# Kernel optimization log

Measured on AMD Instinct MI355X. Metric: run time of the kernel, lower is better.

The kernel has to match this reference:

```python
import jax, jax.numpy as jnp
import numpy as np

VOCAB = 50257
D = 1024
EDGES = [0, 20000, 40000, VOCAB]  # cluster boundaries
HSZ = [1024, 256, 64]             # D // 4**i per cluster


def setup_inputs() -> dict:
    key = jax.random.key(0)
    ks = jax.random.split(key, 8)
    emb_input = jax.random.randint(ks[0], (8, 2048), 0, VOCAB, dtype=jnp.int64)
    inp = {"emb_input": emb_input}
    for i in range(3):
        vsz = EDGES[i + 1] - EDGES[i]
        h = HSZ[i]
        inp[f"emb{i}"] = jax.random.normal(ks[1 + 2 * i], (vsz, h), dtype=jnp.float32) * 0.02
        # nn.Linear(h, D, bias=False) weight has shape [D, h]
        inp[f"w{i}"] = jax.random.normal(ks[2 + 2 * i], (D, h), dtype=jnp.float32) * 0.02
    return inp


def reference(emb_input, emb0, w0, emb1, w1, emb2, w2):
    B, S = emb_input.shape
    idx = emb_input.reshape(-1)  # [N]
    clusters = [(emb0, w0), (emb1, w1), (emb2, w2)]
    out = jnp.zeros((idx.shape[0], D), dtype=jnp.float32)
    for i, (emb, w) in enumerate(clusters):
        lo, hi = EDGES[i], EDGES[i + 1]
        mask = (idx >= lo) & (idx < hi)                       # [N]
        local = jnp.clip(idx - lo, 0, emb.shape[0] - 1)       # in-range gather ids
        h = emb[local]                                        # [N, hsz_i]
        proj = jnp.einsum('nh,dh->nd', h, w)                  # [N, D]
        out = out + jnp.where(mask[:, None], proj, 0.0)
    return out.reshape(B, S, D)
```

## Files before the change

### kernel.cpp

```cpp
#include <hip/hip_runtime.h>
#include <hip/hip_bf16.h>
#include <stdint.h>

#define DOUT 1024
#define NMAX 16384

#define BM 256
#define BN 128
#define LDSBUF 49152
#define BOFFS 32768

typedef __attribute__((ext_vector_type(8))) short short8;
typedef __attribute__((ext_vector_type(4))) float floatx4;

__device__ __forceinline__ unsigned short f2bf(float f) {
  union { float f; uint32_t u; } v;
  v.f = f;
  return (unsigned short)((v.u + 0x7FFFu + ((v.u >> 16) & 1u)) >> 16);
}

__device__ __forceinline__ short8 cvt8(float4 a, float4 b) {
  __hip_bfloat162 p0 = __float22bfloat162_rn(make_float2(a.x, a.y));
  __hip_bfloat162 p1 = __float22bfloat162_rn(make_float2(a.z, a.w));
  __hip_bfloat162 p2 = __float22bfloat162_rn(make_float2(b.x, b.y));
  __hip_bfloat162 p3 = __float22bfloat162_rn(make_float2(b.z, b.w));
  union { __hip_bfloat162 h[4]; short8 s; } u;
  u.h[0] = p0; u.h[1] = p1; u.h[2] = p2; u.h[3] = p3;
  return u.s;
}

__global__ __launch_bounds__(256) void classify_cvt_kernel(
    const int* __restrict__ idx, int* __restrict__ cnt,
    int* __restrict__ bucket, int* __restrict__ blocal, int N,
    const float* __restrict__ w0, const float* __restrict__ w1,
    const float* __restrict__ w2, unsigned short* __restrict__ wb0,
    unsigned short* __restrict__ wb1, unsigned short* __restrict__ wb2) {
  if (blockIdx.x < 64) {
    int n = blockIdx.x * 256 + threadIdx.x;
    int lane = threadIdx.x & 63;
    int c = -1, v = 0;
    if (n < N) {
      v = idx[n];
      c = (v < 20000) ? 0 : ((v < 40000) ? 1 : 2);
    }
#pragma unroll
    for (int k = 0; k < 3; ++k) {
      unsigned long long m = __ballot(c == k);
      if (c == k) {
        int leader = __ffsll((unsigned long long)m) - 1;
        int base = 0;
        if (lane == leader) base = atomicAdd(&cnt[k], (int)__popcll(m));
        base = __shfl(base, leader);
        int rank = (int)__popcll(m & ((1ull << (unsigned)lane) - 1ull));
        int lo = (k == 0) ? 0 : (k == 1) ? 20000 : 40000;
        bucket[k * NMAX + base + rank] = n;
        blocal[k * NMAX + base + rank] = v - lo;
      }
    }
  } else {
    int i = (blockIdx.x - 64) * 256 + threadIdx.x;
    if (i >= 344064) return;
    const float4* src;
    ushort4* dst;
    if (i < 262144) {
      src = (const float4*)w0 + i;
      dst = (ushort4*)wb0 + i;
    } else if (i < 327680) {
      src = (const float4*)w1 + (i - 262144);
      dst = (ushort4*)wb1 + (i - 262144);
    } else {
      src = (const float4*)w2 + (i - 327680);
      dst = (ushort4*)wb2 + (i - 327680);
    }
    float4 v = *src;
    ushort4 o;
    o.x = f2bf(v.x); o.y = f2bf(v.y); o.z = f2bf(v.z); o.w = f2bf(v.w);
    *dst = o;
  }
}

__global__ __launch_bounds__(256) void gather_kernel(
    const float* __restrict__ emb0, const float* __restrict__ emb1,
    const float* __restrict__ emb2, const int* __restrict__ cnt,
    const int* __restrict__ blocal, unsigned short* __restrict__ Abf) {
  const int b = blockIdx.x;
  const int c0 = cnt[0], c1 = cnt[1], c2 = cnt[2];
  const float* emb;
  const int* bl;
  int H, count, baseRow, lg;
  size_t off;
  if (b < 4096) {
    emb = emb0; bl = blocal; H = 1024; count = c0; off = 0;
    baseRow = b * 4; lg = 6;
  } else if (b < 5120) {
    emb = emb1; bl = blocal + NMAX; H = 256; count = c1;
    off = (size_t)c0 * 1024; baseRow = (b - 4096) * 16; lg = 4;
  } else {
    emb = emb2; bl = blocal + 2 * NMAX; H = 64; count = c2;
    off = (size_t)c0 * 1024 + (size_t)c1 * 256; baseRow = (b - 5120) * 64; lg = 2;
  }
  const int tid = threadIdx.x;
  const int r = baseRow + (tid >> lg);
  if (r >= count) return;
  const int e = (tid & ((1 << lg) - 1)) * 16;
  const float* src = emb + (size_t)bl[r] * H + e;
  unsigned short* d = Abf + off + (size_t)r * H + e;
  float4 v0 = ((const float4*)src)[0];
  float4 v1 = ((const float4*)src)[1];
  float4 v2 = ((const float4*)src)[2];
  float4 v3 = ((const float4*)src)[3];
  *(short8*)d = cvt8(v0, v1);
  *(short8*)(d + 8) = cvt8(v2, v3);
}

template <int H>
__device__ __forceinline__ void gemm_body(
    const unsigned short* __restrict__ A, const unsigned short* __restrict__ B,
    int count, const int* __restrict__ bucket, float* __restrict__ out,
    char* lds, int* rowTok) {
  const int m0 = blockIdx.y * BM;
  if (m0 >= count) return;
  const int n0 = blockIdx.x * BN;
  constexpr int NT = H / 64;

  const int tid = threadIdx.x;
  const int wave = tid >> 6;
  const int lane = tid & 63;
  const int quad = lane >> 4;
  const int l16 = lane & 15;
  const int wm = wave & 3;
  const int wn = wave >> 2;

  if (tid < BM) {
    int m = m0 + tid;
    rowTok[tid] = (m < count) ? bucket[m] : -1;
  }

  const int dl = wave * 1024 + lane * 16;
  const int lswz = dl ^ (((dl >> 7) & 3) << 4);
  const int rW = lswz >> 6;
  const int ckW = (lswz >> 4) & 3;
  const char* Abyte = (const char*)A;
  const char* Bbyte = (const char*)B;
  const size_t aOff0 = ((size_t)(m0 + rW) * H) * 2 + ckW * 16;
  const size_t aOff1 = ((size_t)(m0 + 128 + rW) * H) * 2 + ckW * 16;
  const size_t bOff = ((size_t)(n0 + rW) * H) * 2 + ckW * 16;

  auto stage = [&](int kt, char* buf) {
    const int kb = kt * 128;
#pragma unroll
    for (int s = 0; s < 2; ++s) {
      __builtin_amdgcn_global_load_lds(
          (const __attribute__((address_space(1))) void*)(Abyte + aOff0 + kb + s * 64),
          (__attribute__((address_space(3))) void*)(buf + s * 16384 + wave * 1024),
          16, 0, 0);
      __builtin_amdgcn_global_load_lds(
          (const __attribute__((address_space(1))) void*)(Abyte + aOff1 + kb + s * 64),
          (__attribute__((address_space(3))) void*)(buf + s * 16384 + 8192 + wave * 1024),
          16, 0, 0);
      __builtin_amdgcn_global_load_lds(
          (const __attribute__((address_space(1))) void*)(Bbyte + bOff + kb + s * 64),
          (__attribute__((address_space(3))) void*)(buf + BOFFS + s * 8192 + wave * 1024),
          16, 0, 0);
    }
  };

  int offA[2][4], offB[2][4];
#pragma unroll
  for (int s = 0; s < 2; ++s) {
#pragma unroll
    for (int i = 0; i < 4; ++i) {
      int ba = (wm * 64 + i * 16 + l16) * 64 + quad * 16;
      offA[s][i] = s * 16384 + (ba ^ (((ba >> 7) & 3) << 4));
      int bb = (wn * 64 + i * 16 + l16) * 64 + quad * 16;
      offB[s][i] = BOFFS + s * 8192 + (bb ^ (((bb >> 7) & 3) << 4));
    }
  }

  if (NT >= 1) stage(0, lds);
  if (NT >= 2) stage(1, lds + LDSBUF);
  if (NT >= 3) stage(2, lds + 2 * LDSBUF);

  floatx4 acc[4][4];
#pragma unroll
  for (int i = 0; i < 4; ++i)
#pragma unroll
    for (int j = 0; j < 4; ++j) acc[i][j] = (floatx4){0.f, 0.f, 0.f, 0.f};

#pragma unroll
  for (int kt = 0; kt < NT; ++kt) {
    const int rem = NT - 1 - kt;
    if (rem >= 2)
      asm volatile("s_waitcnt vmcnt(12)" ::: "memory");
    else if (rem == 1)
      asm volatile("s_waitcnt vmcnt(6)" ::: "memory");
    else
      asm volatile("s_waitcnt vmcnt(0)" ::: "memory");
    asm volatile("s_barrier" ::: "memory");

    const char* buf = lds + (kt % 3) * LDSBUF;
#pragma unroll
    for (int ph = 0; ph < 4; ++ph) {
      const int mh = ph >> 1, nh = ph & 1;
      short8 a[2][2], b[2][2];
#pragma unroll
      for (int s = 0; s < 2; ++s)
#pragma unroll
        for (int i = 0; i < 2; ++i) {
          a[s][i] = *(const short8*)(buf + offA[s][mh * 2 + i]);
          b[s][i] = *(const short8*)(buf + offB[s][nh * 2 + i]);
        }
      __builtin_amdgcn_s_setprio(1);
#pragma unroll
      for (int s = 0; s < 2; ++s)
#pragma unroll
        for (int i = 0; i < 2; ++i)
#pragma unroll
          for (int j = 0; j < 2; ++j)
            acc[mh * 2 + i][nh * 2 + j] = __builtin_amdgcn_mfma_f32_16x16x32_bf16(
                a[s][i], b[s][j], acc[mh * 2 + i][nh * 2 + j], 0, 0, 0);
      __builtin_amdgcn_s_setprio(0);
    }
    asm volatile("s_barrier" ::: "memory");
    if (kt + 3 < NT) stage(kt + 3, lds + (kt % 3) * LDSBUF);
  }

  const int colBase = n0 + wn * 64 + l16;
#pragma unroll
  for (int mi = 0; mi < 4; ++mi) {
#pragma unroll
    for (int r = 0; r < 4; ++r) {
      int tok = rowTok[wm * 64 + mi * 16 + quad * 4 + r];
      if (tok >= 0) {
        float* o = out + (size_t)tok * DOUT + colBase;
#pragma unroll
        for (int ni = 0; ni < 4; ++ni) o[ni * 16] = acc[mi][ni][r];
      }
    }
  }
}

__global__ __launch_bounds__(512, 2) void gemm_pipe(
    const unsigned short* __restrict__ Abf,
    const unsigned short* __restrict__ wb0,
    const unsigned short* __restrict__ wb1,
    const unsigned short* __restrict__ wb2, const int* __restrict__ cnt,
    const int* __restrict__ bucket, float* __restrict__ out) {
  __shared__ __align__(16) char lds[3 * LDSBUF + BM * 4];
  int* rowTok = (int*)(lds + 3 * LDSBUF);

  const int z = blockIdx.z;
  const int c0 = cnt[0];
  const int c1 = cnt[1];
  if (z == 0)
    gemm_body<1024>(Abf, wb0, c0, bucket, out, lds, rowTok);
  else if (z == 1)
    gemm_body<256>(Abf + (size_t)c0 * 1024, wb1, c1, bucket + NMAX, out, lds,
                   rowTok);
  else
    gemm_body<64>(Abf + (size_t)c0 * 1024 + (size_t)c1 * 256, wb2, cnt[2],
                  bucket + 2 * NMAX, out, lds, rowTok);
}

extern "C" void kernel_launch(void* const* d_in, const int* in_sizes, int n_in,
                              void* d_out, int out_size, void* d_ws, size_t ws_size,
                              hipStream_t stream) {
  const int* idx = (const int*)d_in[0];
  const float* emb0 = (const float*)d_in[1];
  const float* w0 = (const float*)d_in[2];
  const float* emb1 = (const float*)d_in[3];
  const float* w1 = (const float*)d_in[4];
  const float* emb2 = (const float*)d_in[5];
  const float* w2 = (const float*)d_in[6];
  float* out = (float*)d_out;
  const int N = in_sizes[0];

  char* ws = (char*)d_ws;
  int* cnt = (int*)ws;
  int* bucket = (int*)(ws + 1024);
  int* blocal = bucket + 3 * NMAX;
  size_t off = 1024 + (size_t)6 * NMAX * 4;
  off = (off + 255) & ~(size_t)255;
  unsigned short* wb0 = (unsigned short*)(ws + off); off += (size_t)DOUT * 1024 * 2;
  unsigned short* wb1 = (unsigned short*)(ws + off); off += (size_t)DOUT * 256 * 2;
  unsigned short* wb2 = (unsigned short*)(ws + off); off += (size_t)DOUT * 64 * 2;
  off = (off + 255) & ~(size_t)255;
  unsigned short* Abf = (unsigned short*)(ws + off);
  off += (size_t)(NMAX + 256) * 1024 * 2;

  hipMemsetAsync(cnt, 0, 16 * sizeof(int), stream);

  classify_cvt_kernel<<<64 + 1344, 256, 0, stream>>>(
      idx, cnt, bucket, blocal, N, w0, w1, w2, wb0, wb1, wb2);

  gather_kernel<<<5376, 256, 0, stream>>>(emb0, emb1, emb2, cnt, blocal, Abf);

  dim3 grid(DOUT / BN, NMAX / BM, 3);
  gemm_pipe<<<grid, 512, 0, stream>>>(Abf, wb0, wb1, wb2, cnt, bucket, out);
}
```

Baseline: 197.7 us.

## Coalesce gather-convert loads, swizzle GEMM workgroup order, load all fragments before MFMAs

The gather/convert kernel now has each thread handle four strided float4 chunks instead of one contiguous 64-byte chunk, so neighbouring lanes read neighbouring addresses. The GEMM remaps its linear workgroup id so consecutive ids are spread across eight XCD groups, aiming for better L2 locality. The inner k-loop also loads all A/B fragments for the whole tile at once and then issues all 32 MFMAs in one prioritised block, replacing four phased load/compute steps. This raises register pressure and gives up LDS/MFMA interleaving. The remap assumes the workgroup count divides evenly by eight.

```diff
diff --git a/kernel.cpp b/kernel.cpp
--- a/kernel.cpp
+++ b/kernel.cpp
@@ -19,13 +19,11 @@
   return (unsigned short)((v.u + 0x7FFFu + ((v.u >> 16) & 1u)) >> 16);
 }
 
-__device__ __forceinline__ short8 cvt8(float4 a, float4 b) {
-  __hip_bfloat162 p0 = __float22bfloat162_rn(make_float2(a.x, a.y));
-  __hip_bfloat162 p1 = __float22bfloat162_rn(make_float2(a.z, a.w));
-  __hip_bfloat162 p2 = __float22bfloat162_rn(make_float2(b.x, b.y));
-  __hip_bfloat162 p3 = __float22bfloat162_rn(make_float2(b.z, b.w));
-  union { __hip_bfloat162 h[4]; short8 s; } u;
-  u.h[0] = p0; u.h[1] = p1; u.h[2] = p2; u.h[3] = p3;
+__device__ __forceinline__ ushort4 cvt4(float4 v) {
+  __hip_bfloat162 p0 = __float22bfloat162_rn(make_float2(v.x, v.y));
+  __hip_bfloat162 p1 = __float22bfloat162_rn(make_float2(v.z, v.w));
+  union { __hip_bfloat162 h[2]; ushort4 s; } u;
+  u.h[0] = p0; u.h[1] = p1;
   return u.s;
 }
 
@@ -102,15 +100,16 @@
   const int tid = threadIdx.x;
   const int r = baseRow + (tid >> lg);
   if (r >= count) return;
-  const int e = (tid & ((1 << lg) - 1)) * 16;
+  const int tpr = 1 << lg;
+  const int e = (tid & (tpr - 1)) * 4;
+  const int stride = tpr * 4;
   const float* src = emb + (size_t)bl[r] * H + e;
   unsigned short* d = Abf + off + (size_t)r * H + e;
-  float4 v0 = ((const float4*)src)[0];
-  float4 v1 = ((const float4*)src)[1];
-  float4 v2 = ((const float4*)src)[2];
-  float4 v3 = ((const float4*)src)[3];
-  *(short8*)d = cvt8(v0, v1);
-  *(short8*)(d + 8) = cvt8(v2, v3);
+#pragma unroll
+  for (int j = 0; j < 4; ++j) {
+    float4 v = *(const float4*)(src + j * stride);
+    *(ushort4*)(d + j * stride) = cvt4(v);
+  }
 }
 
 template <int H>
@@ -118,9 +117,16 @@
     const unsigned short* __restrict__ A, const unsigned short* __restrict__ B,
     int count, const int* __restrict__ bucket, float* __restrict__ out,
     char* lds, int* rowTok) {
-  const int m0 = blockIdx.y * BM;
+  const int nwg = gridDim.x * gridDim.y;
+  const int orig = blockIdx.y * gridDim.x + blockIdx.x;
+  const int q = nwg >> 3;
+  const int wg = (orig & 7) * q + (orig >> 3);
+  const int bx = wg % gridDim.x;
+  const int by = wg / gridDim.x;
+
+  const int m0 = by * BM;
   if (m0 >= count) return;
-  const int n0 = blockIdx.x * BN;
+  const int n0 = bx * BN;
   constexpr int NT = H / 64;
 
   const int tid = threadIdx.x;
@@ -199,28 +205,24 @@
     asm volatile("s_barrier" ::: "memory");
 
     const char* buf = lds + (kt % 3) * LDSBUF;
-#pragma unroll
-    for (int ph = 0; ph < 4; ++ph) {
-      const int mh = ph >> 1, nh = ph & 1;
-      short8 a[2][2], b[2][2];
-#pragma unroll
-      for (int s = 0; s < 2; ++s)
-#pragma unroll
-        for (int i = 0; i < 2; ++i) {
-          a[s][i] = *(const short8*)(buf + offA[s][mh * 2 + i]);
-          b[s][i] = *(const short8*)(buf + offB[s][nh * 2 + i]);
-        }
-      __builtin_amdgcn_s_setprio(1);
-#pragma unroll
-      for (int s = 0; s < 2; ++s)
-#pragma unroll
-        for (int i = 0; i < 2; ++i)
-#pragma unroll
-          for (int j = 0; j < 2; ++j)
-            acc[mh * 2 + i][nh * 2 + j] = __builtin_amdgcn_mfma_f32_16x16x32_bf16(
-                a[s][i], b[s][j], acc[mh * 2 + i][nh * 2 + j], 0, 0, 0);
-      __builtin_amdgcn_s_setprio(0);
-    }
+    short8 a[2][4], b[2][4];
+#pragma unroll
+    for (int s = 0; s < 2; ++s)
+#pragma unroll
+      for (int i = 0; i < 4; ++i) {
+        a[s][i] = *(const short8*)(buf + offA[s][i]);
+        b[s][i] = *(const short8*)(buf + offB[s][i]);
+      }
+    __builtin_amdgcn_s_setprio(1);
+#pragma unroll
+    for (int s = 0; s < 2; ++s)
+#pragma unroll
+      for (int i = 0; i < 4; ++i)
+#pragma unroll
+        for (int j = 0; j < 4; ++j)
+          acc[i][j] = __builtin_amdgcn_mfma_f32_16x16x32_bf16(
+              a[s][i], b[s][j], acc[i][j], 0, 0, 0);
+    __builtin_amdgcn_s_setprio(0);
     asm volatile("s_barrier" ::: "memory");
     if (kt + 3 < NT) stage(kt + 3, lds + (kt % 3) * LDSBUF);
   }
```

Result: slower. 233.8 us (+18.2%).
